# Optimization experiments

Measured on AMD Instinct MI355X. Metric: run time of the kernel, lower is better.

The kernel has to match this reference:

```python
import jax, jax.numpy as jnp
import numpy as np

REF_CHANNEL = 0
DIAG_EPS = 1e-7   # diagonal loading coefficient
EPS = 1e-8        # denominator stabilizer in MVDR
PSD_EPS = 1e-15   # mask-normalization eps in PSD
B, F, C, T = 4, 1025, 6, 1000


def setup_inputs() -> dict:
    key = jax.random.key(0)
    k1, k2, k3, k4 = jax.random.split(key, 4)
    return {
        "spec_real": jax.random.normal(k1, (B, F, C, T), jnp.float32),
        "spec_imag": jax.random.normal(k2, (B, F, C, T), jnp.float32),
        "mask_s": jax.random.uniform(k3, (B, F, T), jnp.float32),
        "mask_n": jax.random.uniform(k4, (B, F, T), jnp.float32),
    }


def _psd(X, mask):
    # PSD module with normalize=True: normalize mask over time, then
    # psd = sum_t mask[t] * X[:,t] X[:,t]^H  -> (..., freq, C, C)
    # Fused einsum avoids the (B,F,T,C,C) intermediate the torch code builds.
    m = mask / (jnp.sum(mask, axis=-1, keepdims=True) + PSD_EPS)
    return jnp.einsum('bfct,bfet,bft->bfce', X, jnp.conj(X), m.astype(X.dtype))


def _tik_reg(psd):
    # psd + (diag_eps * trace(psd).real + eps) * I
    c = psd.shape[-1]
    tr = jnp.trace(psd, axis1=-2, axis2=-1).real
    epsilon = tr * DIAG_EPS + EPS
    return psd + epsilon[..., None, None] * jnp.eye(c, dtype=psd.dtype)


def reference(spec_real, spec_imag, mask_s, mask_n):
    X = jax.lax.complex(spec_real, spec_imag)          # (B,F,C,T) complex64
    psd_s = _psd(X, mask_s)                            # (B,F,C,C)
    psd_n = _tik_reg(_psd(X, mask_n))                  # diagonal loading
    numerator = jnp.linalg.solve(psd_n, psd_s)         # batched 6x6 complex solve
    tr = jnp.trace(numerator, axis1=-2, axis2=-1)      # complex trace
    ws = numerator / (tr[..., None, None] + EPS)       # (B,F,C,C)
    # einsum('...fec,...c->...fe', ws, onehot(ref)) == select ref column
    w = ws[..., REF_CHANNEL]                           # (B,F,C)
    # apply beamforming: sum_c conj(w)[c] * X[c,t]
    out = jnp.einsum('bfc,bfct->bft', jnp.conj(w), X)  # (B,F,T) complex64
    return out
```

## Files before the change

kernel.cpp:

```cpp
#include <hip/hip_runtime.h>

constexpr int kB = 4;
constexpr int kF = 1025;
constexpr int kC = 6;
constexpr int kT = 1000;
constexpr int NPAIR = 15;
constexpr int NACCG = 37;
constexpr int THREADS = 256;

__global__ __launch_bounds__(THREADS)
void mvdr_kernel(const float* __restrict__ spec_real,
                 const float* __restrict__ spec_imag,
                 const float* __restrict__ mask_s,
                 const float* __restrict__ mask_n,
                 float* __restrict__ out,
                 int spec_elems, int mask_elems, int out_elems) {
  const int bf   = blockIdx.x;
  const int tid  = threadIdx.x;
  const int lane = tid & 63;
  const int wave = tid >> 6;
  const int grp  = tid >> 7;
  const int gtid = tid & 127;

  __shared__ __align__(16) float sXr[kC * kT];
  __shared__ __align__(16) float sXi[kC * kT];
  __shared__ float sRed[4 * NACCG];
  __shared__ float sFin[74];
  __shared__ float sW[2 * kC];

  const size_t sbase = (size_t)bf * (kC * kT);
  const size_t mbase = (size_t)bf * kT;

  const bool spec_ok = (sbase + (size_t)(kC * kT)) <= (size_t)spec_elems;
  const bool mask_ok = (mbase + (size_t)kT) <= (size_t)mask_elems;

  if (spec_ok) {
    const float4* gr4 = reinterpret_cast<const float4*>(spec_real + sbase);
    const float4* gi4 = reinterpret_cast<const float4*>(spec_imag + sbase);
    float4* lr4 = reinterpret_cast<float4*>(sXr);
    float4* li4 = reinterpret_cast<float4*>(sXi);
    for (int i = tid; i < (kC * kT) / 4; i += THREADS) {
      lr4[i] = gr4[i];
      li4[i] = gi4[i];
    }
  } else {
    for (int i = tid; i < kC * kT; i += THREADS) { sXr[i] = 0.f; sXi[i] = 0.f; }
  }
  __syncthreads();

  const float* __restrict__ mptr = (grp == 0) ? mask_s : mask_n;

  float acc[NACCG];
#pragma unroll
  for (int j = 0; j < NACCG; ++j) acc[j] = 0.f;

  for (int t = gtid; t < kT; t += 128) {
    float xr[kC], xi[kC];
#pragma unroll
    for (int c = 0; c < kC; ++c) {
      xr[c] = sXr[c * kT + t];
      xi[c] = sXi[c * kT + t];
    }
    float m = mask_ok ? mptr[mbase + t] : 0.f;
    acc[36] += m;
#pragma unroll
    for (int c = 0; c < kC; ++c) {
      float p = xr[c] * xr[c] + xi[c] * xi[c];
      acc[c] += m * p;
    }
    int k = 0;
#pragma unroll
    for (int c = 0; c < kC; ++c) {
#pragma unroll
      for (int e = c + 1; e < kC; ++e) {
        float pr = xr[c] * xr[e] + xi[c] * xi[e];
        float pi = xi[c] * xr[e] - xr[c] * xi[e];
        acc[6  + k] += m * pr;
        acc[21 + k] += m * pi;
        ++k;
      }
    }
  }

#pragma unroll
  for (int j = 0; j < NACCG; ++j) {
    float v = acc[j];
#pragma unroll
    for (int off = 32; off > 0; off >>= 1)
      v += __shfl_down(v, off, 64);
    if (lane == 0) sRed[wave * NACCG + j] = v;
  }
  __syncthreads();
  if (tid < NACCG) {
    float s = sRed[tid]             + sRed[NACCG + tid];
    float n = sRed[2 * NACCG + tid] + sRed[3 * NACCG + tid];
    if (tid < 36) {
      sFin[tid]      = s;
      sFin[36 + tid] = n;
    } else {
      sFin[72] = s;
      sFin[73] = n;
    }
  }
  __syncthreads();

  if (tid == 0) {
    float isS = 1.f / (sFin[72] + 1e-15f);
    float isN = 1.f / (sFin[73] + 1e-15f);

    float trN = 0.f;
#pragma unroll
    for (int c = 0; c < kC; ++c) trN += sFin[36 + c];
    trN *= isN;
    float epsl = trN * 1e-7f + 1e-8f;

    float Sr[kC][kC], Si[kC][kC];
    float Ar[kC][kC], Ai[kC][kC];
#pragma unroll
    for (int c = 0; c < kC; ++c) {
      Sr[c][c] = sFin[c] * isS;             Si[c][c] = 0.f;
      Ar[c][c] = sFin[36 + c] * isN + epsl; Ai[c][c] = 0.f;
    }
    {
      int k = 0;
#pragma unroll
      for (int c = 0; c < kC; ++c) {
#pragma unroll
        for (int e = c + 1; e < kC; ++e) {
          float spr = sFin[6  + k] * isS, spi = sFin[21 + k] * isS;
          Sr[c][e] = spr;  Si[c][e] = spi;
          Sr[e][c] = spr;  Si[e][c] = -spi;
          float npr = sFin[42 + k] * isN, npi = sFin[57 + k] * isN;
          Ar[c][e] = npr;  Ai[c][e] = npi;
          Ar[e][c] = npr;  Ai[e][c] = -npi;
          ++k;
        }
      }
    }

    float invd[kC];
#pragma unroll
    for (int j = 0; j < kC; ++j) {
      float d = Ar[j][j];
#pragma unroll
      for (int k2 = 0; k2 < j; ++k2)
        d -= Ar[j][k2] * Ar[j][k2] + Ai[j][k2] * Ai[j][k2];
      d = fmaxf(d, 1e-30f);
      float ljj = sqrtf(d);
      float inv = 1.f / ljj;
      Ar[j][j] = ljj;
      invd[j] = inv;
#pragma unroll
      for (int i = j + 1; i < kC; ++i) {
        float re = Ar[i][j], im = Ai[i][j];
#pragma unroll
        for (int k2 = 0; k2 < j; ++k2) {
          re -= Ar[i][k2] * Ar[j][k2] + Ai[i][k2] * Ai[j][k2];
          im -= Ai[i][k2] * Ar[j][k2] - Ar[i][k2] * Ai[j][k2];
        }
        Ar[i][j] = re * inv;
        Ai[i][j] = im * inv;
      }
    }

    float trR = 0.f, trI = 0.f;
    float w0r[kC], w0i[kC];
#pragma unroll
    for (int m = 0; m < kC; ++m) {
      float yr[kC], yi[kC];
#pragma unroll
      for (int i = 0; i < kC; ++i) {
        float re = Sr[i][m], im = Si[i][m];
#pragma unroll
        for (int k2 = 0; k2 < i; ++k2) {
          re -= Ar[i][k2] * yr[k2] - Ai[i][k2] * yi[k2];
          im -= Ar[i][k2] * yi[k2] + Ai[i][k2] * yr[k2];
        }
        yr[i] = re * invd[i];
        yi[i] = im * invd[i];
      }
#pragma unroll
      for (int i = kC - 1; i >= 0; --i) {
        float re = yr[i], im = yi[i];
#pragma unroll
        for (int k2 = i + 1; k2 < kC; ++k2) {
          re -= Ar[k2][i] * yr[k2] + Ai[k2][i] * yi[k2];
          im -= Ar[k2][i] * yi[k2] - Ai[k2][i] * yr[k2];
        }
        yr[i] = re * invd[i];
        yi[i] = im * invd[i];
      }
      trR += yr[m];
      trI += yi[m];
      if (m == 0) {
#pragma unroll
        for (int c = 0; c < kC; ++c) { w0r[c] = yr[c]; w0i[c] = yi[c]; }
      }
    }

    float dr = trR + 1e-8f, di = trI;
    float idn = 1.f / (dr * dr + di * di);
#pragma unroll
    for (int c = 0; c < kC; ++c) {
      sW[2 * c]     = (w0r[c] * dr + w0i[c] * di) * idn;
      sW[2 * c + 1] = (w0i[c] * dr - w0r[c] * di) * idn;
    }
  }
  __syncthreads();

  float wr[kC], wi[kC];
#pragma unroll
  for (int c = 0; c < kC; ++c) {
    wr[c] = sW[2 * c];
    wi[c] = sW[2 * c + 1];
  }
  const size_t plane = (size_t)kB * kF * kT;
  for (int t = tid; t < kT; t += THREADS) {
    float o_r = 0.f, o_i = 0.f;
#pragma unroll
    for (int c = 0; c < kC; ++c) {
      float xr = sXr[c * kT + t];
      float xi = sXi[c * kT + t];
      o_r += wr[c] * xr + wi[c] * xi;
      o_i += wr[c] * xi - wi[c] * xr;
    }
    size_t idx = (size_t)bf * kT + t;
    if (idx < (size_t)out_elems)         out[idx]         = o_r;
    if (idx + plane < (size_t)out_elems) out[idx + plane] = o_i;
  }
}

extern "C" void kernel_launch(void* const* d_in, const int* in_sizes, int n_in,
                              void* d_out, int out_size, void* d_ws, size_t ws_size,
                              hipStream_t stream) {
  const float* spec[2] = {nullptr, nullptr};
  const float* mask[2] = {nullptr, nullptr};
  int ns = 0, nm = 0;
  for (int i = 0; i < n_in; ++i) {
    if (in_sizes[i] == kB * kF * kC * kT) { if (ns < 2) spec[ns++] = (const float*)d_in[i]; }
    else if (in_sizes[i] == kB * kF * kT) { if (nm < 2) mask[nm++] = (const float*)d_in[i]; }
  }
  const float* spec_real = spec[0] ? spec[0] : (const float*)d_in[0];
  const float* spec_imag = spec[1] ? spec[1] : (const float*)d_in[1];
  const float* mask_s    = mask[0] ? mask[0] : (const float*)d_in[2];
  const float* mask_n    = mask[1] ? mask[1] : (const float*)d_in[3];

  int spec_elems = kB * kF * kC * kT;
  int mask_elems = kB * kF * kT;

  dim3 grid(kB * kF);
  dim3 block(THREADS);
  hipLaunchKernelGGL(mvdr_kernel, grid, block, 0, stream,
                     spec_real, spec_imag, mask_s, mask_n,
                     (float*)d_out, spec_elems, mask_elems, out_size);
}
```

Before: 364.6 us.

## Split MVDR into PSD, batched solve, and beamform kernels via workspace

```diff
diff --git a/kernel.cpp b/kernel.cpp
--- a/kernel.cpp
+++ b/kernel.cpp
@@ -4,9 +4,236 @@
 constexpr int kF = 1025;
 constexpr int kC = 6;
 constexpr int kT = 1000;
-constexpr int NPAIR = 15;
+constexpr int kBF = kB * kF;
 constexpr int NACCG = 37;
 constexpr int THREADS = 256;
+constexpr int PSD_STRIDE = 80;
+constexpr int W_STRIDE = 16;
+
+__global__ __launch_bounds__(THREADS)
+void psd_kernel(const float* __restrict__ spec_real,
+                const float* __restrict__ spec_imag,
+                const float* __restrict__ mask_s,
+                const float* __restrict__ mask_n,
+                float* __restrict__ ws_psd,
+                int spec_elems, int mask_elems) {
+  const int bf   = blockIdx.x;
+  const int tid  = threadIdx.x;
+  const int lane = tid & 63;
+  const int wave = tid >> 6;
+  const int grp  = tid >> 7;
+  const int gtid = tid & 127;
+
+  __shared__ float sRed[4 * NACCG];
+
+  const size_t sbase = (size_t)bf * (kC * kT);
+  const size_t mbase = (size_t)bf * kT;
+  const bool spec_ok = (sbase + (size_t)(kC * kT)) <= (size_t)spec_elems;
+  const bool mask_ok = (mbase + (size_t)kT) <= (size_t)mask_elems;
+
+  const float* __restrict__ mptr = (grp == 0) ? mask_s : mask_n;
+  const float* __restrict__ xrb = spec_real + sbase;
+  const float* __restrict__ xib = spec_imag + sbase;
+
+  float acc[NACCG];
+#pragma unroll
+  for (int j = 0; j < NACCG; ++j) acc[j] = 0.f;
+
+  for (int t = gtid; t < kT; t += 128) {
+    float xr[kC], xi[kC];
+#pragma unroll
+    for (int c = 0; c < kC; ++c) {
+      xr[c] = spec_ok ? xrb[c * kT + t] : 0.f;
+      xi[c] = spec_ok ? xib[c * kT + t] : 0.f;
+    }
+    float m = mask_ok ? mptr[mbase + t] : 0.f;
+    acc[36] += m;
+#pragma unroll
+    for (int c = 0; c < kC; ++c) {
+      float p = xr[c] * xr[c] + xi[c] * xi[c];
+      acc[c] += m * p;
+    }
+    int k = 0;
+#pragma unroll
+    for (int c = 0; c < kC; ++c) {
+#pragma unroll
+      for (int e = c + 1; e < kC; ++e) {
+        float pr = xr[c] * xr[e] + xi[c] * xi[e];
+        float pi = xi[c] * xr[e] - xr[c] * xi[e];
+        acc[6  + k] += m * pr;
+        acc[21 + k] += m * pi;
+        ++k;
+      }
+    }
+  }
+
+#pragma unroll
+  for (int j = 0; j < NACCG; ++j) {
+    float v = acc[j];
+#pragma unroll
+    for (int off = 32; off > 0; off >>= 1)
+      v += __shfl_down(v, off, 64);
+    if (lane == 0) sRed[wave * NACCG + j] = v;
+  }
+  __syncthreads();
+  if (tid < NACCG) {
+    float s = sRed[tid]             + sRed[NACCG + tid];
+    float n = sRed[2 * NACCG + tid] + sRed[3 * NACCG + tid];
+    float* wsbf = ws_psd + (size_t)bf * PSD_STRIDE;
+    wsbf[tid]      = s;
+    wsbf[40 + tid] = n;
+  }
+}
+
+__global__ __launch_bounds__(64)
+void solve_kernel(const float* __restrict__ ws_psd,
+                  float* __restrict__ ws_w, int nbf) {
+  const int bf = blockIdx.x * 64 + threadIdx.x;
+  if (bf >= nbf) return;
+  const float* f = ws_psd + (size_t)bf * PSD_STRIDE;
+  float isS = 1.f / (f[36] + 1e-15f);
+  float isN = 1.f / (f[76] + 1e-15f);
+
+  float trN = 0.f;
+#pragma unroll
+  for (int c = 0; c < kC; ++c) trN += f[40 + c];
+  trN *= isN;
+  float epsl = trN * 1e-7f + 1e-8f;
+
+  float Sr[kC][kC], Si[kC][kC];
+  float Ar[kC][kC], Ai[kC][kC];
+#pragma unroll
+  for (int c = 0; c < kC; ++c) {
+    Sr[c][c] = f[c] * isS;              Si[c][c] = 0.f;
+    Ar[c][c] = f[40 + c] * isN + epsl;  Ai[c][c] = 0.f;
+  }
+  {
+    int k = 0;
+#pragma unroll
+    for (int c = 0; c < kC; ++c) {
+#pragma unroll
+      for (int e = c + 1; e < kC; ++e) {
+        float spr = f[6  + k] * isS, spi = f[21 + k] * isS;
+        Sr[c][e] = spr;  Si[c][e] = spi;
+        Sr[e][c] = spr;  Si[e][c] = -spi;
+        float npr = f[46 + k] * isN, npi = f[61 + k] * isN;
+        Ar[c][e] = npr;  Ai[c][e] = npi;
+        Ar[e][c] = npr;  Ai[e][c] = -npi;
+        ++k;
+      }
+    }
+  }
+
+  float invd[kC];
+#pragma unroll
+  for (int j = 0; j < kC; ++j) {
+    float d = Ar[j][j];
+#pragma unroll
+    for (int k2 = 0; k2 < j; ++k2)
+      d -= Ar[j][k2] * Ar[j][k2] + Ai[j][k2] * Ai[j][k2];
+    d = fmaxf(d, 1e-30f);
+    float ljj = sqrtf(d);
+    float inv = 1.f / ljj;
+    Ar[j][j] = ljj;
+    invd[j] = inv;
+#pragma unroll
+    for (int i = j + 1; i < kC; ++i) {
+      float re = Ar[i][j], im = Ai[i][j];
+#pragma unroll
+      for (int k2 = 0; k2 < j; ++k2) {
+        re -= Ar[i][k2] * Ar[j][k2] + Ai[i][k2] * Ai[j][k2];
+        im -= Ai[i][k2] * Ar[j][k2] - Ar[i][k2] * Ai[j][k2];
+      }
+      Ar[i][j] = re * inv;
+      Ai[i][j] = im * inv;
+    }
+  }
+
+  float trR = 0.f, trI = 0.f;
+  float w0r[kC], w0i[kC];
+#pragma unroll
+  for (int m = 0; m < kC; ++m) {
+    float yr[kC], yi[kC];
+#pragma unroll
+    for (int i = 0; i < kC; ++i) {
+      float re = Sr[i][m], im = Si[i][m];
+#pragma unroll
+      for (int k2 = 0; k2 < i; ++k2) {
+        re -= Ar[i][k2] * yr[k2] - Ai[i][k2] * yi[k2];
+        im -= Ar[i][k2] * yi[k2] + Ai[i][k2] * yr[k2];
+      }
+      yr[i] = re * invd[i];
+      yi[i] = im * invd[i];
+    }
+#pragma unroll
+    for (int i = kC - 1; i >= 0; --i) {
+      float re = yr[i], im = yi[i];
+#pragma unroll
+      for (int k2 = i + 1; k2 < kC; ++k2) {
+        re -= Ar[k2][i] * yr[k2] + Ai[k2][i] * yi[k2];
+        im -= Ar[k2][i] * yi[k2] - Ai[k2][i] * yr[k2];
+      }
+      yr[i] = re * invd[i];
+      yi[i] = im * invd[i];
+    }
+    trR += yr[m];
+    trI += yi[m];
+    if (m == 0) {
+#pragma unroll
+      for (int c = 0; c < kC; ++c) { w0r[c] = yr[c]; w0i[c] = yi[c]; }
+    }
+  }
+
+  float dr = trR + 1e-8f, di = trI;
+  float idn = 1.f / (dr * dr + di * di);
+  float* w = ws_w + (size_t)bf * W_STRIDE;
+#pragma unroll
+  for (int c = 0; c < kC; ++c) {
+    w[2 * c]     = (w0r[c] * dr + w0i[c] * di) * idn;
+    w[2 * c + 1] = (w0i[c] * dr - w0r[c] * di) * idn;
+  }
+}
+
+__global__ __launch_bounds__(THREADS)
+void bf_kernel(const float* __restrict__ spec_real,
+               const float* __restrict__ spec_imag,
+               const float* __restrict__ ws_w,
+               float* __restrict__ out,
+               int spec_elems, int out_elems) {
+  const int bf  = blockIdx.x;
+  const int tid = threadIdx.x;
+
+  __shared__ float sW[2 * kC];
+  if (tid < 2 * kC) sW[tid] = ws_w[(size_t)bf * W_STRIDE + tid];
+  __syncthreads();
+
+  float wr[kC], wi[kC];
+#pragma unroll
+  for (int c = 0; c < kC; ++c) {
+    wr[c] = sW[2 * c];
+    wi[c] = sW[2 * c + 1];
+  }
+
+  const size_t sbase = (size_t)bf * (kC * kT);
+  const bool spec_ok = (sbase + (size_t)(kC * kT)) <= (size_t)spec_elems;
+  const float* __restrict__ xrb = spec_real + sbase;
+  const float* __restrict__ xib = spec_imag + sbase;
+  const size_t plane = (size_t)kB * kF * kT;
+
+  for (int t = tid; t < kT; t += THREADS) {
+    float o_r = 0.f, o_i = 0.f;
+#pragma unroll
+    for (int c = 0; c < kC; ++c) {
+      float xr = spec_ok ? xrb[c * kT + t] : 0.f;
+      float xi = spec_ok ? xib[c * kT + t] : 0.f;
+      o_r += wr[c] * xr + wi[c] * xi;
+      o_i += wr[c] * xi - wi[c] * xr;
+    }
+    size_t idx = (size_t)bf * kT + t;
+    if (idx < (size_t)out_elems)         out[idx]         = o_r;
+    if (idx + plane < (size_t)out_elems) out[idx + plane] = o_i;
+  }
+}
 
 __global__ __launch_bounds__(THREADS)
 void mvdr_kernel(const float* __restrict__ spec_real,
@@ -30,7 +257,6 @@
 
   const size_t sbase = (size_t)bf * (kC * kT);
   const size_t mbase = (size_t)bf * kT;
-
   const bool spec_ok = (sbase + (size_t)(kC * kT)) <= (size_t)spec_elems;
   const bool mask_ok = (mbase + (size_t)kT) <= (size_t)mask_elems;
 
@@ -49,7 +275,6 @@
   __syncthreads();
 
   const float* __restrict__ mptr = (grp == 0) ? mask_s : mask_n;
-
   float acc[NACCG];
 #pragma unroll
   for (int j = 0; j < NACCG; ++j) acc[j] = 0.f;
@@ -107,7 +332,6 @@
   if (tid == 0) {
     float isS = 1.f / (sFin[72] + 1e-15f);
     float isN = 1.f / (sFin[73] + 1e-15f);
-
     float trN = 0.f;
 #pragma unroll
     for (int c = 0; c < kC; ++c) trN += sFin[36 + c];
@@ -248,9 +472,23 @@
   int spec_elems = kB * kF * kC * kT;
   int mask_elems = kB * kF * kT;
 
-  dim3 grid(kB * kF);
-  dim3 block(THREADS);
-  hipLaunchKernelGGL(mvdr_kernel, grid, block, 0, stream,
-                     spec_real, spec_imag, mask_s, mask_n,
-                     (float*)d_out, spec_elems, mask_elems, out_size);
+  const size_t need = (size_t)kBF * (PSD_STRIDE + W_STRIDE) * sizeof(float);
+  if (d_ws != nullptr && ws_size >= need) {
+    float* ws_psd = (float*)d_ws;
+    float* ws_w   = ws_psd + (size_t)kBF * PSD_STRIDE;
+    hipLaunchKernelGGL(psd_kernel, dim3(kBF), dim3(THREADS), 0, stream,
+                       spec_real, spec_imag, mask_s, mask_n,
+                       ws_psd, spec_elems, mask_elems);
+    hipLaunchKernelGGL(solve_kernel, dim3((kBF + 63) / 64), dim3(64), 0, stream,
+                       ws_psd, ws_w, kBF);
+    hipLaunchKernelGGL(bf_kernel, dim3(kBF), dim3(THREADS), 0, stream,
+                       spec_real, spec_imag, ws_w,
+                       (float*)d_out, spec_elems, out_size);
+  } else {
+    dim3 grid(kBF);
+    dim3 block(THREADS);
+    hipLaunchKernelGGL(mvdr_kernel, grid, block, 0, stream,
+                       spec_real, spec_imag, mask_s, mask_n,
+                       (float*)d_out, spec_elems, mask_elems, out_size);
+  }
 }
```

New measurement: 295.7 us. 1.23x faster.
